# Kernel optimization log

Measured on AMD Instinct MI355X. Metric: run time of the kernel, lower is better.

Reference implementation:

```python
import jax, jax.numpy as jnp
import numpy as np

N_NODES = 100000
N_EDGES = 3200000
IN_FEATS = 16
OUT_FEATS = 2
K = 3


def setup_inputs() -> dict:
    key = jax.random.key(0)
    k1, k2, k3, k4 = jax.random.split(key, 4)
    in_feat = jax.random.normal(k1, (N_NODES, IN_FEATS), dtype=jnp.float32)
    # Linear(K*in_feats -> out_feats, bias=False) weight, torch layout (out, in)
    W = jax.random.normal(k2, (OUT_FEATS, K * IN_FEATS), dtype=jnp.float32) * (1.0 / np.sqrt(K * IN_FEATS))
    src = jax.random.randint(k3, (N_EDGES,), 0, N_NODES, dtype=jnp.int64)
    dst = jax.random.randint(k4, (N_EDGES,), 0, N_NODES, dtype=jnp.int64)
    # cached dgl.laplacian_lambda_max value; 2.0 is the normalized-Laplacian bound
    lambda_max = jnp.full((1,), 2.0, dtype=jnp.float32)
    return {"in_feat": in_feat, "W": W, "src": src, "dst": dst, "lambda_max": lambda_max}


def reference(in_feat, W, src, dst, lambda_max):
    N = in_feat.shape[0]
    # in-degree based symmetric normalization, clamp(min=1)
    deg = jax.ops.segment_sum(jnp.ones_like(dst, dtype=in_feat.dtype), dst, num_segments=N)
    norm = jnp.clip(deg, 1.0) ** -0.5  # (N,)
    norm = norm[:, None]
    re_norm = (2.0 / lambda_max)[None, :]  # (1,1), broadcasts over nodes

    def prop(x):
        # D^{-1/2} A D^{-1/2} x via gather from src, scatter-sum to dst
        m = (x * norm)[src]                                    # (E, d)
        return jax.ops.segment_sum(m, dst, num_segments=N) * norm

    X0 = in_feat
    X1 = -re_norm * prop(X0) + X0 * (re_norm - 1.0)
    X2 = -2.0 * re_norm * prop(X1) + X1 * (2.0 * (re_norm - 1.0)) - X0
    Xt = jnp.concatenate([X0, X1, X2], axis=1)                 # (N, K*d)
    h = Xt @ W.T                                               # (N, out)
    return jax.nn.relu(h)  # DGL ChebConv default activation
```

## Files before the change

### kernel.cpp

```cpp
#include <hip/hip_runtime.h>
#include <hip/hip_bf16.h>


#define NN   100000
#define NE   3200000
#define F    16
#define CB   128
#define NBUK 782
#define ECHK 8192
#define NBLK 391
#define LCAP 5632
#define HXW  1025
#define PCAP 4608

__device__ __forceinline__ float bflo(unsigned int u) {
    return __uint_as_float(u << 16);
}
__device__ __forceinline__ float bfhi(unsigned int u) {
    return __uint_as_float(u & 0xffff0000u);
}
__device__ __forceinline__ unsigned int f2bf(float f) {
    __hip_bfloat16 b = __float2bfloat16(f);
    return (unsigned int)*reinterpret_cast<unsigned short*>(&b);
}

__global__ __launch_bounds__(512) void k_lsort(const int* __restrict__ src,
        const int* __restrict__ dst, int* __restrict__ hxg, int* __restrict__ csort) {
    __shared__ int pk[ECHK];
    __shared__ int hx[HXW];
    __shared__ int cur[1024];
    __shared__ int csum[512];
    int t = threadIdx.x, blk = blockIdx.x;
    for (int j = t; j < 1024; j += 512) hx[j] = 0;
    __syncthreads();
    int s0 = blk * ECHK;
    int lim = min(s0 + ECHK, NE);
    for (int e = s0 + t; e < lim; e += 512)
        atomicAdd(&hx[dst[e] >> 7], 1);
    __syncthreads();
    int b0 = t * 2;
    int c0 = hx[b0], c1 = hx[b0 + 1];
    csum[t] = c0 + c1;
    __syncthreads();
    for (int o = 1; o < 512; o <<= 1) {
        int add = (t >= o) ? csum[t - o] : 0;
        __syncthreads();
        csum[t] += add;
        __syncthreads();
    }
    int ce = csum[t] - (c0 + c1);
    hx[b0] = ce;  hx[b0 + 1] = ce + c0;
    cur[b0] = ce; cur[b0 + 1] = ce + c0;
    if (t == 511) hx[1024] = csum[511];
    __syncthreads();
    for (int j = t; j < HXW; j += 512)
        hxg[blk * HXW + j] = hx[j];
    for (int e = s0 + t; e < lim; e += 512) {
        int d = dst[e];
        int pos = atomicAdd(&cur[d >> 7], 1);
        pk[pos] = (src[e] << 7) | (d & 127);
    }
    __syncthreads();
    int len = lim - s0;
    for (int i = t; i < len; i += 512)
        csort[s0 + i] = pk[i];
}

__global__ __launch_bounds__(512) void k_sort(const int* __restrict__ csort,
        const int* __restrict__ hxg, const float* __restrict__ X0,
        int* __restrict__ es, unsigned int* __restrict__ P,
        unsigned short* __restrict__ Y0, unsigned short* __restrict__ Y1) {
    __shared__ int pk2[LCAP];
    __shared__ int cnt[CB], loc[CB], cur[CB];
    __shared__ float nvs[CB];
    int b = blockIdx.x, t = threadIdx.x;
    if (t < CB) cnt[t] = 0;
    if (b == 0 && t < 4) {
        ((uint2*)Y0)[(size_t)NN * 4 + t] = make_uint2(0u, 0u);
        ((uint2*)Y1)[(size_t)NN * 4 + t] = make_uint2(0u, 0u);
    }
    int h0 = 0, rl = 0;
    if (t < NBLK) {
        h0 = hxg[t * HXW + b];
        rl = hxg[t * HXW + b + 1] - h0;
    }
    int sbase = t * ECHK + h0;
    __syncthreads();
    for (int i = 0; i < rl; ++i) {
        int p = csort[sbase + i];
        atomicAdd(&cnt[p & 127], 1);
    }
    __syncthreads();
    int pc = 0;
    if (t < CB) { pc = (cnt[t] + 7) & ~7; loc[t] = pc; }
    __syncthreads();
    for (int o = 1; o < CB; o <<= 1) {
        int add = 0;
        if (t < CB && t >= o) add = loc[t - o];
        __syncthreads();
        if (t < CB) loc[t] += add;
        __syncthreads();
    }
    if (t < CB) {
        int excl = loc[t] - pc;
        loc[t] = excl;
        cur[t] = excl;
        int n = b * CB + t;
        if (n < NN) {
            unsigned dgc = cnt[t] > 1023 ? 1023u : (unsigned)cnt[t];
            P[n] = ((unsigned)((b * LCAP + excl) >> 3) << 10) | dgc;
            nvs[t] = rsqrtf((float)(cnt[t] < 1 ? 1 : cnt[t]));
        }
    }
    __syncthreads();
    int plen = loc[CB - 1] + ((cnt[CB - 1] + 7) & ~7);
    if (plen > LCAP) plen = LCAP;
    if (t < CB) {
        int e0 = loc[t] + cnt[t];
        int e1 = loc[t] + ((cnt[t] + 7) & ~7);
        for (int i = e0; i < e1 && i < LCAP; ++i) pk2[i] = NN;
    }
    for (int i = 0; i < rl; ++i) {
        int p = csort[sbase + i];
        int pos = atomicAdd(&cur[p & 127], 1);
        if (pos < LCAP) pk2[pos] = p >> 7;
    }
    for (int j = t; j < CB * 4; j += 512) {
        int dl = j >> 2;
        int n = b * CB + dl;
        if (n < NN) {
            float nv = nvs[dl];
            size_t g4 = (size_t)n * 4 + (j & 3);
            float4 x0 = ((const float4*)X0)[g4];
            uint2 o;
            o.x = f2bf(x0.x * nv) | (f2bf(x0.y * nv) << 16);
            o.y = f2bf(x0.z * nv) | (f2bf(x0.w * nv) << 16);
            ((uint2*)Y0)[g4] = o;
        }
    }
    __syncthreads();
    for (int i = t; i < plen; i += 512)
        es[b * LCAP + i] = pk2[i];
}

__global__ __launch_bounds__(256) void k_prop1(const unsigned int* __restrict__ P,
        const int* __restrict__ es, const unsigned short* __restrict__ Y0,
        const float* __restrict__ X0, const float* __restrict__ lm,
        unsigned short* __restrict__ Y1) {
    __shared__ __align__(16) int sidx[PCAP];
    int blk = blockIdx.x, t = threadIdx.x;
    int b = blk >> 1, half = blk & 1;
    int n0 = b * CB + half * 64;
    if (n0 >= NN) return;
    unsigned pk0 = P[n0];
    int nL = min(n0 + 63, NN - 1);
    unsigned pkL = P[nL];
    int st = (int)(pk0 >> 10) << 3;
    int en = ((int)(pkL >> 10) << 3) + (int)(((pkL & 1023u) + 7u) & ~7u);
    int slen = en - st;
    if (slen > PCAP) slen = PCAP;
    for (int i = t; i < slen; i += 256)
        sidx[i] = es[st + i];
    __syncthreads();
    int n = n0 + (t >> 2), h = t & 3;
    if (n >= NN) return;
    unsigned pkn = P[n];
    int beg = ((int)(pkn >> 10) << 3) - st;
    int dg = (int)(pkn & 1023u);
    int nb = (dg + 7) >> 3;
    const uint2* Yv = (const uint2*)Y0;
    float a0 = 0.f, a1 = 0.f, a2 = 0.f, a3 = 0.f;
    for (int bb = 0; bb < nb; ++bb) {
        int e0 = beg + bb * 8;
        int4 ia = *(const int4*)&sidx[e0];
        int4 ib = *(const int4*)&sidx[e0 + 4];
#define ACC(S) { uint2 u = Yv[(size_t)(S) * 4 + h]; \
                 a0 += bflo(u.x); a1 += bfhi(u.x); \
                 a2 += bflo(u.y); a3 += bfhi(u.y); }
        ACC(ia.x) ACC(ia.y) ACC(ia.z) ACC(ia.w)
        ACC(ib.x) ACC(ib.y) ACC(ib.z) ACC(ib.w)
    }
    float nv = rsqrtf((float)(dg < 1 ? 1 : dg));
    float r  = 2.0f / lm[0];
    float k1 = -r * nv, k2 = r - 1.0f;
    int tid4 = n * 4 + h;
    float4 x0 = ((const float4*)X0)[tid4];
    float x1a = k1 * a0 + k2 * x0.x;
    float x1b = k1 * a1 + k2 * x0.y;
    float x1c = k1 * a2 + k2 * x0.z;
    float x1d = k1 * a3 + k2 * x0.w;
    uint2 o;
    o.x = f2bf(nv * x1a) | (f2bf(nv * x1b) << 16);
    o.y = f2bf(nv * x1c) | (f2bf(nv * x1d) << 16);
    ((uint2*)Y1)[tid4] = o;
}

__global__ __launch_bounds__(256) void k_prop2(const unsigned int* __restrict__ P,
        const int* __restrict__ es, const unsigned short* __restrict__ Y1,
        const float* __restrict__ X0, const float* __restrict__ lm,
        const float* __restrict__ W, float* __restrict__ out) {
    __shared__ __align__(16) int sidx[PCAP];
    __shared__ float Ws[96];
    int blk = blockIdx.x, t = threadIdx.x;
    int b = blk >> 1, half = blk & 1;
    int n0 = b * CB + half * 64;
    if (n0 >= NN) return;
    if (t < 96) Ws[t] = W[t];
    unsigned pk0 = P[n0];
    int nL = min(n0 + 63, NN - 1);
    unsigned pkL = P[nL];
    int st = (int)(pk0 >> 10) << 3;
    int en = ((int)(pkL >> 10) << 3) + (int)(((pkL & 1023u) + 7u) & ~7u);
    int slen = en - st;
    if (slen > PCAP) slen = PCAP;
    for (int i = t; i < slen; i += 256)
        sidx[i] = es[st + i];
    __syncthreads();
    int n = n0 + (t >> 2), h = t & 3;
    if (n >= NN) return;
    unsigned pkn = P[n];
    int beg = ((int)(pkn >> 10) << 3) - st;
    int dg = (int)(pkn & 1023u);
    int nb = (dg + 7) >> 3;
    const uint2* Yv = (const uint2*)Y1;
    float a0 = 0.f, a1 = 0.f, a2 = 0.f, a3 = 0.f;
    for (int bb = 0; bb < nb; ++bb) {
        int e0 = beg + bb * 8;
        int4 ia = *(const int4*)&sidx[e0];
        int4 ib = *(const int4*)&sidx[e0 + 4];
        ACC(ia.x) ACC(ia.y) ACC(ia.z) ACC(ia.w)
        ACC(ib.x) ACC(ib.y) ACC(ib.z) ACC(ib.w)
    }
    int dc = dg < 1 ? 1 : dg;
    float nv = rsqrtf((float)dc);
    float rn = sqrtf((float)dc);
    float r  = 2.0f / lm[0];
    int tid4 = n * 4 + h;
    float4 x0 = ((const float4*)X0)[tid4];
    uint2 uy = ((const uint2*)Y1)[tid4];
    float x1a = bflo(uy.x) * rn, x1b = bfhi(uy.x) * rn;
    float x1c = bflo(uy.y) * rn, x1d = bfhi(uy.y) * rn;
    float c1 = -2.0f * r * nv, c2 = 2.0f * (r - 1.0f);
    float x2a = c1 * a0 + c2 * x1a - x0.x;
    float x2b = c1 * a1 + c2 * x1b - x0.y;
    float x2c = c1 * a2 + c2 * x1c - x0.z;
    float x2d = c1 * a3 + c2 * x1d - x0.w;
    int f0 = 4 * h;
    float t0 = Ws[f0] * x0.x + Ws[f0 + 1] * x0.y + Ws[f0 + 2] * x0.z + Ws[f0 + 3] * x0.w
             + Ws[16 + f0] * x1a + Ws[17 + f0] * x1b + Ws[18 + f0] * x1c + Ws[19 + f0] * x1d
             + Ws[32 + f0] * x2a + Ws[33 + f0] * x2b + Ws[34 + f0] * x2c + Ws[35 + f0] * x2d;
    float t1 = Ws[48 + f0] * x0.x + Ws[49 + f0] * x0.y + Ws[50 + f0] * x0.z + Ws[51 + f0] * x0.w
             + Ws[64 + f0] * x1a + Ws[65 + f0] * x1b + Ws[66 + f0] * x1c + Ws[67 + f0] * x1d
             + Ws[80 + f0] * x2a + Ws[81 + f0] * x2b + Ws[82 + f0] * x2c + Ws[83 + f0] * x2d;
    t0 += __shfl_xor(t0, 2, 4); t0 += __shfl_xor(t0, 1, 4);
    t1 += __shfl_xor(t1, 2, 4); t1 += __shfl_xor(t1, 1, 4);
    if (h == 0) {
        out[(size_t)n * 2 + 0] = fmaxf(t0, 0.f);
        out[(size_t)n * 2 + 1] = fmaxf(t1, 0.f);
    }
}

extern "C" void kernel_launch(void* const* d_in, const int* in_sizes, int n_in,
                              void* d_out, int out_size, void* d_ws, size_t ws_size,
                              hipStream_t stream) {
    const float* X0  = (const float*)d_in[0];
    const float* W   = (const float*)d_in[1];
    const int*   src = (const int*)d_in[2];
    const int*   dst = (const int*)d_in[3];
    const float* lm  = (const float*)d_in[4];
    float* out = (float*)d_out;

    int*   hxg   = (int*)d_ws;
    int*   csort = hxg + (size_t)NBLK * HXW;
    int*   es    = csort + NE;
    unsigned int* P = (unsigned int*)(es + (size_t)NBUK * LCAP);
    unsigned short* Y0 = (unsigned short*)(P + NN);
    unsigned short* Y1 = Y0 + (size_t)(NN + 1) * F;

    k_lsort<<<NBLK, 512, 0, stream>>>(src, dst, hxg, csort);
    k_sort <<<NBUK, 512, 0, stream>>>(csort, hxg, X0, es, P, Y0, Y1);
    k_prop1<<<NBUK * 2, 256, 0, stream>>>(P, es, Y0, X0, lm, Y1);
    k_prop2<<<NBUK * 2, 256, 0, stream>>>(P, es, Y1, X0, lm, W, out);
}
```

Before: 190.1 us.

## Stage bucket edge runs into LDS with coalesced loads in k_sort

k_sort previously had each of 391 threads walk its own run of csort serially, issuing uncoalesced scalar global loads twice (once for counting, once for placement). The new code prefix-sums the run lengths, has 16-lane groups copy each run contiguously into a shared buffer, and then does both counting and placement passes over LDS with all 512 threads. This removes the load imbalance and the repeated global reads, at the cost of an extra LDS buffer of LCAP ints (lowering occupancy) and a 512-wide scan.

```diff
diff --git a/kernel.cpp b/kernel.cpp
--- a/kernel.cpp
+++ b/kernel.cpp
@@ -70,26 +70,50 @@
         const int* __restrict__ hxg, const float* __restrict__ X0,
         int* __restrict__ es, unsigned int* __restrict__ P,
         unsigned short* __restrict__ Y0, unsigned short* __restrict__ Y1) {
+    __shared__ int pk[LCAP];
     __shared__ int pk2[LCAP];
+    __shared__ int dsc[512];
+    __shared__ int hS[NBLK];
+    __shared__ short rls[NBLK];
     __shared__ int cnt[CB], loc[CB], cur[CB];
     __shared__ float nvs[CB];
     int b = blockIdx.x, t = threadIdx.x;
+    int h0 = 0, rl = 0;
+    if (t < NBLK) {
+        h0 = hxg[t * HXW + b];
+        rl = hxg[t * HXW + b + 1] - h0;
+        hS[t] = h0;
+        rls[t] = (short)(rl > 4096 ? 4096 : rl);
+    }
+    dsc[t] = rl;
     if (t < CB) cnt[t] = 0;
     if (b == 0 && t < 4) {
         ((uint2*)Y0)[(size_t)NN * 4 + t] = make_uint2(0u, 0u);
         ((uint2*)Y1)[(size_t)NN * 4 + t] = make_uint2(0u, 0u);
     }
-    int h0 = 0, rl = 0;
-    if (t < NBLK) {
-        h0 = hxg[t * HXW + b];
-        rl = hxg[t * HXW + b + 1] - h0;
-    }
-    int sbase = t * ECHK + h0;
-    __syncthreads();
-    for (int i = 0; i < rl; ++i) {
-        int p = csort[sbase + i];
-        atomicAdd(&cnt[p & 127], 1);
-    }
+    __syncthreads();
+    for (int o = 1; o < 512; o <<= 1) {
+        int add = (t >= o) ? dsc[t - o] : 0;
+        __syncthreads();
+        dsc[t] += add;
+        __syncthreads();
+    }
+    int len = dsc[511];
+    if (len > LCAP) len = LCAP;
+    int g = t >> 4, lane = t & 15;
+    for (int c = g; c < NBLK; c += 32) {
+        int rlc = rls[c];
+        if (rlc == 0) continue;
+        int dpos = dsc[c] - rlc;
+        if (dpos >= LCAP) continue;
+        if (dpos + rlc > LCAP) rlc = LCAP - dpos;
+        int sb = c * ECHK + hS[c];
+        for (int l = lane; l < rlc; l += 16)
+            pk[dpos + l] = csort[sb + l];
+    }
+    __syncthreads();
+    for (int i = t; i < len; i += 512)
+        atomicAdd(&cnt[pk[i] & 127], 1);
     __syncthreads();
     int pc = 0;
     if (t < CB) { pc = (cnt[t] + 7) & ~7; loc[t] = pc; }
@@ -120,8 +144,8 @@
         int e1 = loc[t] + ((cnt[t] + 7) & ~7);
         for (int i = e0; i < e1 && i < LCAP; ++i) pk2[i] = NN;
     }
-    for (int i = 0; i < rl; ++i) {
-        int p = csort[sbase + i];
+    for (int i = t; i < len; i += 512) {
+        int p = pk[i];
         int pos = atomicAdd(&cur[p & 127], 1);
         if (pos < LCAP) pk2[pos] = p >> 7;
     }
```

Measured after the change: 171.0 us. -10.1%, faster.
